# Kernel tuning notes

Hardware: AMD Instinct MI355X
Metric: run time of the kernel (lower is better)

The kernel has to match this reference:

```python
import jax, jax.numpy as jnp
import numpy as np

K = 3
PAD = 1

def conv2d(x, w, b=None):
    # x: [B,C,H,W], w: [O,C,kh,kw], stride 1, padding 1
    y = jax.lax.conv_general_dilated(x, w, (1, 1), [(PAD, PAD), (PAD, PAD)],
                                     dimension_numbers=('NCHW', 'OIHW', 'NCHW'))
    if b is not None:
        y = y + b[None, :, None, None]
    return y

def deform_conv2d(x, offset, mask, w):
    # Faithful torchvision DeformConv2d (v2, stride=1, dilation=1, pad=1, no bias).
    # x: [B,C,H,W]; offset: [B,2*K*K,H,W] with (dy,dx) interleaved per kernel pt;
    # mask: [B,K*K,H,W]; w: [O,C,K,K]
    B, C, H, W = x.shape
    KK = K * K
    off = offset.reshape(B, KK, 2, H, W)
    offs_y, offs_x = off[:, :, 0], off[:, :, 1]           # [B,KK,H,W]
    ky = (jnp.arange(KK) // K).astype(jnp.float32) - PAD   # kernel row offsets
    kx = (jnp.arange(KK) % K).astype(jnp.float32) - PAD    # kernel col offsets
    py = offs_y + jnp.arange(H, dtype=jnp.float32)[None, None, :, None] + ky[None, :, None, None]
    px = offs_x + jnp.arange(W, dtype=jnp.float32)[None, None, None, :] + kx[None, :, None, None]
    y0f = jnp.floor(py); x0f = jnp.floor(px)
    wy = py - y0f; wx = px - x0f                           # bilinear fractions
    y0 = y0f.astype(jnp.int32); x0 = x0f.astype(jnp.int32)
    xf = x.reshape(B, C, H * W)

    def corner(yi, xi):
        valid = ((yi >= 0) & (yi < H) & (xi >= 0) & (xi < W)).astype(x.dtype)
        idx = jnp.clip(yi, 0, H - 1) * W + jnp.clip(xi, 0, W - 1)   # [B,KK,H,W]
        g = jax.vmap(lambda img, ix: img[:, ix])(xf, idx.reshape(B, KK * H * W))
        return g.reshape(B, C, KK, H, W) * valid[:, None]

    one = jnp.asarray(1.0, x.dtype)
    samp = (corner(y0, x0)         * ((one - wy) * (one - wx))[:, None]
          + corner(y0, x0 + 1)     * ((one - wy) * wx)[:, None]
          + corner(y0 + 1, x0)     * (wy * (one - wx))[:, None]
          + corner(y0 + 1, x0 + 1) * (wy * wx)[:, None])       # [B,C,KK,H,W]
    if mask is not None:
        samp = samp * mask[:, None]
    O = w.shape[0]
    return jnp.einsum('bckhw,ock->bohw', samp, w.reshape(O, C, KK))

def setup_inputs() -> dict:
    key = jax.random.key(0)
    ks = jax.random.split(key, 7)
    B, C, O, H, W = 4, 64, 64, 128, 128
    x = jax.random.normal(ks[0], (B, C, H, W), jnp.float32)
    ele = jax.random.normal(ks[1], (B, 1, H, W), jnp.float32)
    offset_w = jax.random.normal(ks[2], (2 * K * K, 1, 3, 3), jnp.float32) * 0.1
    offset_b = jnp.zeros((2 * K * K,), jnp.float32)
    mask_w = jax.random.normal(ks[3], (K * K, C, 3, 3), jnp.float32) * (1.0 / np.sqrt(C * 9))
    mask_b = jnp.zeros((K * K,), jnp.float32)
    deform_w = jax.random.normal(ks[4], (O, C, K, K), jnp.float32) * (1.0 / np.sqrt(C * 9))
    return {"x": x, "ele": ele, "offset_w": offset_w, "offset_b": offset_b,
            "mask_w": mask_w, "mask_b": mask_b, "deform_w": deform_w}

def reference(x, ele, offset_w, offset_b, mask_w, mask_b, deform_w):
    offset = conv2d(ele, offset_w, offset_b)                 # [B,18,H,W]
    mask = jax.nn.sigmoid(conv2d(x, mask_w, mask_b))         # [B,9,H,W]
    out = deform_conv2d(x, offset, mask, deform_w)           # [B,O,H,W]
    return jax.nn.relu(out)
```

## Files before the change

### kernel.cpp

```cpp
#include <hip/hip_runtime.h>
#include <hip/hip_bf16.h>
#include <hip/hip_fp16.h>

typedef _Float16 half8 __attribute__((ext_vector_type(8)));
typedef _Float16 half2v __attribute__((ext_vector_type(2)));
typedef float f32x4 __attribute__((ext_vector_type(4)));

#define B_ 4
#define C_ 64
#define O_ 64
#define H_ 128
#define W_ 128
#define HT 8
#define WT 16
#define HALO 3
#define RS 14
#define CS 22

__device__ __forceinline__ unsigned pkh(float lo, float hi) {
  half2v v = {(_Float16)lo, (_Float16)hi};
  return __builtin_bit_cast(unsigned, v);
}

__global__ void build_frags(const float* __restrict__ dw,
                            const float* __restrict__ mw,
                            _Float16* __restrict__ wsb) {
  int t = blockIdx.x * 256 + threadIdx.x;
  if (t < 36864) {
    int j = t & 7, lane = (t >> 3) & 63, ot = (t >> 9) & 3, s = t >> 11;
    int kk = s >> 1, ch = s & 1;
    int o = ot * 16 + (lane & 15);
    int c = ch * 32 + ((lane >> 4) << 3) + j;
    wsb[t] = (_Float16)dw[(o * 64 + c) * 9 + kk];
  } else if (t < 46080) {
    int t2 = t - 36864;
    int j = t2 & 7, lane = (t2 >> 3) & 63, s = t2 >> 9;
    int km = lane & 15;
    int c = (s & 1) * 32 + ((lane >> 4) << 3) + j;
    int tap = s >> 1;
    float v = (km < 9) ? mw[(km * 64 + c) * 9 + tap] : 0.0f;
    wsb[t] = (_Float16)v;
  }
}

__global__ __launch_bounds__(512, 4)
void deform_main(const float* __restrict__ x,
                 const float* __restrict__ ele,
                 const float* __restrict__ ow,
                 const float* __restrict__ ob,
                 const float* __restrict__ mb,
                 const _Float16* __restrict__ wsb,
                 float* __restrict__ out) {
  __shared__ uint4 xs4[RS * CS * 9];
  __shared__ _Float16 offl[128 * 18];
  __shared__ _Float16 maskl[128 * 9];
  __shared__ uint2 cwb[128 * 9];
  __shared__ unsigned crc[128 * 9];

  const int tid = threadIdx.x;
  const int lane = tid & 63;
  const int wv = tid >> 6;
  const int pcl = lane & 15;
  const int lq = lane >> 4;

  const int bid = blockIdx.x;
  const int d = ((bid & 7) << 6) + (bid >> 3);
  const int b = d >> 7;
  const int t7 = d & 127;
  const int r0 = (t7 >> 3) * HT;
  const int c0 = (t7 & 7) * WT;

  float ev[9];
  {
    int tl = tid & 127;
    int pr = tl >> 4, pc = tl & 15;
    int h = r0 + pr, w = c0 + pc;
#pragma unroll
    for (int ty = 0; ty < 3; ++ty)
#pragma unroll
      for (int tx = 0; tx < 3; ++tx) {
        int gy = h - 1 + ty, gx = w - 1 + tx;
        float v = 0.0f;
        if ((unsigned)gy < 128u && (unsigned)gx < 128u)
          v = ele[b * (H_ * W_) + (gy << 7) + gx];
        ev[ty * 3 + tx] = v;
      }
  }

  {
    _Float16* xsb = (_Float16*)xs4;
    const int c2 = tid >> 4;
    const int pl = tid & 15;
    const float* xb0 = x + b * (C_ * H_ * W_) + (2 * c2) * (H_ * W_);
    const float* xb1 = xb0 + (H_ * W_);
    for (int p = pl; p < RS * CS; p += 16) {
      int row = (p * 2979) >> 16;
      int col = p - row * CS;
      int gy = r0 - HALO + row, gx = c0 - HALO + col;
      float v0 = 0.0f, v1 = 0.0f;
      if ((unsigned)gy < 128u && (unsigned)gx < 128u) {
        int gi = (gy << 7) + gx;
        v0 = xb0[gi];
        v1 = xb1[gi];
      }
      half2v hv = {(_Float16)v0, (_Float16)v1};
      *(half2v*)&xsb[p * 72 + 2 * c2] = hv;
    }
  }

  if (tid < 128) {
#pragma unroll
    for (int ci = 0; ci < 18; ++ci) {
      float a = ob[ci];
#pragma unroll
      for (int tap = 0; tap < 9; ++tap) a += ev[tap] * ow[ci * 9 + tap];
      offl[tid * 18 + ci] = (_Float16)a;
    }
  }
  __syncthreads();

  {
    const half8* wfm8 = ((const half8*)wsb) + 4608;
    f32x4 macc = {0.f, 0.f, 0.f, 0.f};
#pragma unroll
    for (int s = 0; s < 18; ++s) {
      const int tap = s >> 1;
      const int chalf = s & 1;
      const int ty = tap / 3, tx = tap - ty * 3;
      half8 aw = wfm8[s * 64 + lane];
      const int csl = chalf * 4 + lq;
      int rc = (wv + (HALO - 1) + ty) * CS + (pcl + (HALO - 1) + tx);
      half8 xv = *(const half8*)(xs4 + rc * 9 + csl);
      macc = __builtin_amdgcn_mfma_f32_16x16x32_f16(aw, xv, macc, 0, 0, 0);
    }
    int px = wv * 16 + pcl;
#pragma unroll
    for (int r = 0; r < 4; ++r) {
      int km = lq * 4 + r;
      if (km < 9) {
        float a = macc[r] + mb[km];
        float m = 1.0f / (1.0f + __expf(-a));
        maskl[px * 9 + km] = (_Float16)m;
      }
    }
  }
  __syncthreads();

  for (int it = tid; it < 128 * 9; it += 512) {
    int px = (it * 7282) >> 16;
    int kk = it - px * 9;
    int pr = px >> 4, pc = px & 15;
    int h = r0 + pr, w = c0 + pc;
    int ky = kk / 3 - 1;
    int kx = kk - (kk / 3) * 3 - 1;
    half2v o2 = *(const half2v*)&offl[px * 18 + kk * 2];
    float m = (float)maskl[px * 9 + kk];
    float py = (float)(h + ky) + (float)o2[0];
    float pxx = (float)(w + kx) + (float)o2[1];
    float fy = floorf(py), fx = floorf(pxx);
    float wy = py - fy, wx = pxx - fx;
    int iy = (int)fy - r0 + HALO;
    int ix = (int)fx - c0 + HALO;
    int vy0 = (unsigned)iy < (unsigned)RS;
    int vy1 = (unsigned)(iy + 1) < (unsigned)RS;
    int vx0 = (unsigned)ix < (unsigned)CS;
    int vx1 = (unsigned)(ix + 1) < (unsigned)CS;
    int cy0 = min(max(iy, 0), RS - 1), cy1 = min(max(iy + 1, 0), RS - 1);
    int cx0 = min(max(ix, 0), CS - 1), cx1 = min(max(ix + 1, 0), CS - 1);
    float wy0 = 1.0f - wy, wx0 = 1.0f - wx;
    float a00 = wy0 * wx0 * m * (float)(vy0 & vx0);
    float a01 = wy0 * wx * m * (float)(vy0 & vx1);
    float a10 = wy * wx0 * m * (float)(vy1 & vx0);
    float a11 = wy * wx * m * (float)(vy1 & vx1);
    int rc00 = cy0 * CS + cx0;
    int drow = (cy1 - cy0) * CS;
    int dcol = cx1 - cx0;
    uint2 cv;
    cv.x = pkh(a00, a01);
    cv.y = pkh(a10, a11);
    cwb[it] = cv;
    crc[it] = (unsigned)rc00 | ((unsigned)drow << 16) | ((unsigned)dcol << 24);
  }
  __syncthreads();

  const half8* wf8 = (const half8*)wsb;
  f32x4 acc[4];
#pragma unroll
  for (int ot = 0; ot < 4; ++ot) {
    f32x4 z = {0.f, 0.f, 0.f, 0.f};
    acc[ot] = z;
  }

  const int px = wv * 16 + pcl;
  const int h = r0 + wv;
  const int w = c0 + pcl;

#pragma unroll
  for (int kk = 0; kk < 9; ++kk) {
    uint2 cv = cwb[px * 9 + kk];
    unsigned rv = crc[px * 9 + kk];
    int rc00 = rv & 0xFFFF;
    int drow = (rv >> 16) & 0xFF;
    int dcol = rv >> 24;
    int rc01 = rc00 + dcol;
    int rc10 = rc00 + drow;
    int rc11 = rc10 + dcol;
    half2v c01 = __builtin_bit_cast(half2v, cv.x);
    half2v c23 = __builtin_bit_cast(half2v, cv.y);
    _Float16 a00 = c01[0], a01 = c01[1], a10 = c23[0], a11 = c23[1];
    half8 a00s = {a00, a00, a00, a00, a00, a00, a00, a00};
    half8 a01s = {a01, a01, a01, a01, a01, a01, a01, a01};
    half8 a10s = {a10, a10, a10, a10, a10, a10, a10, a10};
    half8 a11s = {a11, a11, a11, a11, a11, a11, a11, a11};
#pragma unroll
    for (int ch = 0; ch < 2; ++ch) {
      const int csl = ch * 4 + lq;
      half8 v00 = *(const half8*)(xs4 + rc00 * 9 + csl);
      half8 v01 = *(const half8*)(xs4 + rc01 * 9 + csl);
      half8 v10 = *(const half8*)(xs4 + rc10 * 9 + csl);
      half8 v11 = *(const half8*)(xs4 + rc11 * 9 + csl);
      half8 t = v00 * a00s + v01 * a01s + v10 * a10s + v11 * a11s;
      const int sidx = kk * 2 + ch;
#pragma unroll
      for (int ot = 0; ot < 4; ++ot) {
        half8 bw = wf8[(sidx * 4 + ot) * 64 + lane];
        acc[ot] = __builtin_amdgcn_mfma_f32_16x16x32_f16(bw, t, acc[ot], 0, 0, 0);
      }
    }
  }

#pragma unroll
  for (int ot = 0; ot < 4; ++ot) {
#pragma unroll
    for (int r = 0; r < 4; ++r) {
      int o = ot * 16 + lq * 4 + r;
      float v = fmaxf(acc[ot][r], 0.0f);
      out[((b * O_ + o) << 14) + (h << 7) + w] = v;
    }
  }
}

extern "C" void kernel_launch(void* const* d_in, const int* in_sizes, int n_in,
                              void* d_out, int out_size, void* d_ws, size_t ws_size,
                              hipStream_t stream) {
  const float* x   = (const float*)d_in[0];
  const float* ele = (const float*)d_in[1];
  const float* ow  = (const float*)d_in[2];
  const float* ob  = (const float*)d_in[3];
  const float* mw  = (const float*)d_in[4];
  const float* mb  = (const float*)d_in[5];
  const float* dw  = (const float*)d_in[6];
  _Float16* wsb = (_Float16*)d_ws;

  build_frags<<<180, 256, 0, stream>>>(dw, mw, wsb);
  deform_main<<<512, 512, 0, stream>>>(x, ele, ow, ob, mb, wsb,
                                       (float*)d_out);
}
```

Baseline: 32.29 us.

## Fuse mask sigmoid into bilinear coefficient setup and prefetch weight fragments

Spreads the offset convolution over all 512 threads (4 threads per pixel, each computing a strided subset of the 18 channels) instead of only 128. The mask MFMA epilogue now computes the bilinear corner coefficients directly from the sigmoid in registers, which removes the maskl shared buffer, one barrier and a separate loop. In the main loop, weight fragments for the next step are loaded one step ahead into registers, and s_setprio raises priority around the MFMAs. This costs extra registers under the 512-thread launch bound, and the coefficient work is now limited to 9 of 16 lanes per column group. A leftover empty loop does nothing.

```diff
diff --git a/kernel.cpp b/kernel.cpp
--- a/kernel.cpp
+++ b/kernel.cpp
@@ -53,7 +53,6 @@
                  float* __restrict__ out) {
   __shared__ uint4 xs4[RS * CS * 9];
   __shared__ _Float16 offl[128 * 18];
-  __shared__ _Float16 maskl[128 * 9];
   __shared__ uint2 cwb[128 * 9];
   __shared__ unsigned crc[128 * 9];
 
@@ -72,8 +71,8 @@
 
   float ev[9];
   {
-    int tl = tid & 127;
-    int pr = tl >> 4, pc = tl & 15;
+    int px = tid >> 2;
+    int pr = px >> 4, pc = px & 15;
     int h = r0 + pr, w = c0 + pc;
 #pragma unroll
     for (int ty = 0; ty < 3; ++ty)
@@ -108,13 +107,22 @@
     }
   }
 
-  if (tid < 128) {
+  {
+    int px = tid >> 2;
+    int g = tid & 3;
 #pragma unroll
     for (int ci = 0; ci < 18; ++ci) {
-      float a = ob[ci];
-#pragma unroll
-      for (int tap = 0; tap < 9; ++tap) a += ev[tap] * ow[ci * 9 + tap];
-      offl[tid * 18 + ci] = (_Float16)a;
+      if ((ci & 3) == 0 || (ci - g) % 4 == 0) {}
+    }
+#pragma unroll
+    for (int k5 = 0; k5 < 5; ++k5) {
+      int ci = g + k5 * 4;
+      if (ci < 18) {
+        float a = ob[ci];
+#pragma unroll
+        for (int tap = 0; tap < 9; ++tap) a += ev[tap] * ow[ci * 9 + tap];
+        offl[px * 18 + ci] = (_Float16)a;
+      }
     }
   }
   __syncthreads();
@@ -134,52 +142,44 @@
       macc = __builtin_amdgcn_mfma_f32_16x16x32_f16(aw, xv, macc, 0, 0, 0);
     }
     int px = wv * 16 + pcl;
+    int h = r0 + wv, w = c0 + pcl;
 #pragma unroll
     for (int r = 0; r < 4; ++r) {
-      int km = lq * 4 + r;
-      if (km < 9) {
-        float a = macc[r] + mb[km];
+      int kk = lq * 4 + r;
+      if (kk < 9) {
+        float a = macc[r] + mb[kk];
         float m = 1.0f / (1.0f + __expf(-a));
-        maskl[px * 9 + km] = (_Float16)m;
-      }
-    }
-  }
-  __syncthreads();
-
-  for (int it = tid; it < 128 * 9; it += 512) {
-    int px = (it * 7282) >> 16;
-    int kk = it - px * 9;
-    int pr = px >> 4, pc = px & 15;
-    int h = r0 + pr, w = c0 + pc;
-    int ky = kk / 3 - 1;
-    int kx = kk - (kk / 3) * 3 - 1;
-    half2v o2 = *(const half2v*)&offl[px * 18 + kk * 2];
-    float m = (float)maskl[px * 9 + kk];
-    float py = (float)(h + ky) + (float)o2[0];
-    float pxx = (float)(w + kx) + (float)o2[1];
-    float fy = floorf(py), fx = floorf(pxx);
-    float wy = py - fy, wx = pxx - fx;
-    int iy = (int)fy - r0 + HALO;
-    int ix = (int)fx - c0 + HALO;
-    int vy0 = (unsigned)iy < (unsigned)RS;
-    int vy1 = (unsigned)(iy + 1) < (unsigned)RS;
-    int vx0 = (unsigned)ix < (unsigned)CS;
-    int vx1 = (unsigned)(ix + 1) < (unsigned)CS;
-    int cy0 = min(max(iy, 0), RS - 1), cy1 = min(max(iy + 1, 0), RS - 1);
-    int cx0 = min(max(ix, 0), CS - 1), cx1 = min(max(ix + 1, 0), CS - 1);
-    float wy0 = 1.0f - wy, wx0 = 1.0f - wx;
-    float a00 = wy0 * wx0 * m * (float)(vy0 & vx0);
-    float a01 = wy0 * wx * m * (float)(vy0 & vx1);
-    float a10 = wy * wx0 * m * (float)(vy1 & vx0);
-    float a11 = wy * wx * m * (float)(vy1 & vx1);
-    int rc00 = cy0 * CS + cx0;
-    int drow = (cy1 - cy0) * CS;
-    int dcol = cx1 - cx0;
-    uint2 cv;
-    cv.x = pkh(a00, a01);
-    cv.y = pkh(a10, a11);
-    cwb[it] = cv;
-    crc[it] = (unsigned)rc00 | ((unsigned)drow << 16) | ((unsigned)dcol << 24);
+        int ky = kk / 3 - 1;
+        int kx = kk - (kk / 3) * 3 - 1;
+        half2v o2 = *(const half2v*)&offl[px * 18 + kk * 2];
+        float py = (float)(h + ky) + (float)o2[0];
+        float pxx = (float)(w + kx) + (float)o2[1];
+        float fy = floorf(py), fx = floorf(pxx);
+        float wy = py - fy, wx = pxx - fx;
+        int iy = (int)fy - r0 + HALO;
+        int ix = (int)fx - c0 + HALO;
+        int vy0 = (unsigned)iy < (unsigned)RS;
+        int vy1 = (unsigned)(iy + 1) < (unsigned)RS;
+        int vx0 = (unsigned)ix < (unsigned)CS;
+        int vx1 = (unsigned)(ix + 1) < (unsigned)CS;
+        int cy0 = min(max(iy, 0), RS - 1), cy1 = min(max(iy + 1, 0), RS - 1);
+        int cx0 = min(max(ix, 0), CS - 1), cx1 = min(max(ix + 1, 0), CS - 1);
+        float wy0 = 1.0f - wy, wx0 = 1.0f - wx;
+        float a00 = wy0 * wx0 * m * (float)(vy0 & vx0);
+        float a01 = wy0 * wx * m * (float)(vy0 & vx1);
+        float a10 = wy * wx0 * m * (float)(vy1 & vx0);
+        float a11 = wy * wx * m * (float)(vy1 & vx1);
+        int rc00 = cy0 * CS + cx0;
+        int drow = (cy1 - cy0) * CS;
+        int dcol = cx1 - cx0;
+        uint2 cv;
+        cv.x = pkh(a00, a01);
+        cv.y = pkh(a10, a11);
+        cwb[px * 9 + kk] = cv;
+        crc[px * 9 + kk] = (unsigned)rc00 | ((unsigned)drow << 16) |
+                           ((unsigned)dcol << 24);
+      }
+    }
   }
   __syncthreads();
 
@@ -192,8 +192,10 @@
   }
 
   const int px = wv * 16 + pcl;
-  const int h = r0 + wv;
-  const int w = c0 + pcl;
+
+  half8 bwbuf[4];
+#pragma unroll
+  for (int ot = 0; ot < 4; ++ot) bwbuf[ot] = wf8[ot * 64 + lane];
 
 #pragma unroll
   for (int kk = 0; kk < 9; ++kk) {
@@ -219,16 +221,28 @@
       half8 v01 = *(const half8*)(xs4 + rc01 * 9 + csl);
       half8 v10 = *(const half8*)(xs4 + rc10 * 9 + csl);
       half8 v11 = *(const half8*)(xs4 + rc11 * 9 + csl);
+      const int nsidx = kk * 2 + ch + 1;
+      half8 bwn[4];
+      if (nsidx < 18) {
+#pragma unroll
+        for (int ot = 0; ot < 4; ++ot)
+          bwn[ot] = wf8[(nsidx * 4 + ot) * 64 + lane];
+      }
       half8 t = v00 * a00s + v01 * a01s + v10 * a10s + v11 * a11s;
-      const int sidx = kk * 2 + ch;
-#pragma unroll
-      for (int ot = 0; ot < 4; ++ot) {
-        half8 bw = wf8[(sidx * 4 + ot) * 64 + lane];
-        acc[ot] = __builtin_amdgcn_mfma_f32_16x16x32_f16(bw, t, acc[ot], 0, 0, 0);
-      }
-    }
-  }
-
+      __builtin_amdgcn_s_setprio(1);
+#pragma unroll
+      for (int ot = 0; ot < 4; ++ot)
+        acc[ot] = __builtin_amdgcn_mfma_f32_16x16x32_f16(bwbuf[ot], t, acc[ot], 0, 0, 0);
+      __builtin_amdgcn_s_setprio(0);
+      if (nsidx < 18) {
+#pragma unroll
+        for (int ot = 0; ot < 4; ++ot) bwbuf[ot] = bwn[ot];
+      }
+    }
+  }
+
+  const int h = r0 + wv;
+  const int w = c0 + pcl;
 #pragma unroll
   for (int ot = 0; ot < 4; ++ot) {
 #pragma unroll
```

Result: slower. 33.39 us (+3.4%).

## Split fused deform kernel into coefficient and GEMM kernels via global workspace

Applied to the files above, without the earlier changes.

The single fused kernel is split into two launches. A coefficient kernel computes the mask and bilinear coefficients directly from the mask MFMA outputs and writes them to global workspace. A GEMM kernel then reloads those coefficients into registers and reruns the halo load of x before the deformable MFMA loop. This removes two barriers and some shared-memory use from each kernel, which may improve occupancy. The cost is an extra launch, a second load of the x tile, and a global round-trip of the coefficients.

```diff
diff --git a/kernel.cpp b/kernel.cpp
--- a/kernel.cpp
+++ b/kernel.cpp
@@ -16,6 +16,9 @@
 #define HALO 3
 #define RS 14
 #define CS 22
+
+#define CWG_OFF 92160
+#define CRG_OFF (92160 + 512 * 1152 * 8)
 
 __device__ __forceinline__ unsigned pkh(float lo, float hi) {
   half2v v = {(_Float16)lo, (_Float16)hi};
@@ -44,18 +47,16 @@
 }
 
 __global__ __launch_bounds__(512, 4)
-void deform_main(const float* __restrict__ x,
+void coef_kernel(const float* __restrict__ x,
                  const float* __restrict__ ele,
                  const float* __restrict__ ow,
                  const float* __restrict__ ob,
                  const float* __restrict__ mb,
                  const _Float16* __restrict__ wsb,
-                 float* __restrict__ out) {
+                 uint2* __restrict__ cwg,
+                 unsigned* __restrict__ crg) {
   __shared__ uint4 xs4[RS * CS * 9];
   __shared__ _Float16 offl[128 * 18];
-  __shared__ _Float16 maskl[128 * 9];
-  __shared__ uint2 cwb[128 * 9];
-  __shared__ unsigned crc[128 * 9];
 
   const int tid = threadIdx.x;
   const int lane = tid & 63;
@@ -133,53 +134,111 @@
       half8 xv = *(const half8*)(xs4 + rc * 9 + csl);
       macc = __builtin_amdgcn_mfma_f32_16x16x32_f16(aw, xv, macc, 0, 0, 0);
     }
-    int px = wv * 16 + pcl;
+    const int px = wv * 16 + pcl;
+    const int h = r0 + wv, w = c0 + pcl;
+    const long cbase = (long)d * 1152;
 #pragma unroll
     for (int r = 0; r < 4; ++r) {
-      int km = lq * 4 + r;
-      if (km < 9) {
-        float a = macc[r] + mb[km];
+      int kk = lq * 4 + r;
+      if (kk < 9) {
+        float a = macc[r] + mb[kk];
         float m = 1.0f / (1.0f + __expf(-a));
-        maskl[px * 9 + km] = (_Float16)m;
+        int ky = kk / 3 - 1;
+        int kx = kk - (kk / 3) * 3 - 1;
+        half2v o2 = *(const half2v*)&offl[px * 18 + kk * 2];
+        float py = (float)(h + ky) + (float)o2[0];
+        float pxx = (float)(w + kx) + (float)o2[1];
+        float fy = floorf(py), fx = floorf(pxx);
+        float wy = py - fy, wx = pxx - fx;
+        int iy = (int)fy - r0 + HALO;
+        int ix = (int)fx - c0 + HALO;
+        int vy0 = (unsigned)iy < (unsigned)RS;
+        int vy1 = (unsigned)(iy + 1) < (unsigned)RS;
+        int vx0 = (unsigned)ix < (unsigned)CS;
+        int vx1 = (unsigned)(ix + 1) < (unsigned)CS;
+        int cy0 = min(max(iy, 0), RS - 1), cy1 = min(max(iy + 1, 0), RS - 1);
+        int cx0 = min(max(ix, 0), CS - 1), cx1 = min(max(ix + 1, 0), CS - 1);
+        float wy0 = 1.0f - wy, wx0 = 1.0f - wx;
+        float a00 = wy0 * wx0 * m * (float)(vy0 & vx0);
+        float a01 = wy0 * wx * m * (float)(vy0 & vx1);
+        float a10 = wy * wx0 * m * (float)(vy1 & vx0);
+        float a11 = wy * wx * m * (float)(vy1 & vx1);
+        int rc00 = cy0 * CS + cx0;
+        int drow = (cy1 - cy0) * CS;
+        int dcol = cx1 - cx0;
+        uint2 cv;
+        cv.x = pkh(a00, a01);
+        cv.y = pkh(a10, a11);
+        cwg[cbase + kk * 128 + px] = cv;
+        crg[cbase + kk * 128 + px] =
+            (unsigned)rc00 | ((unsigned)drow << 16) | ((unsigned)dcol << 24);
       }
     }
   }
-  __syncthreads();
-
-  for (int it = tid; it < 128 * 9; it += 512) {
-    int px = (it * 7282) >> 16;
-    int kk = it - px * 9;
-    int pr = px >> 4, pc = px & 15;
-    int h = r0 + pr, w = c0 + pc;
-    int ky = kk / 3 - 1;
-    int kx = kk - (kk / 3) * 3 - 1;
-    half2v o2 = *(const half2v*)&offl[px * 18 + kk * 2];
-    float m = (float)maskl[px * 9 + kk];
-    float py = (float)(h + ky) + (float)o2[0];
-    float pxx = (float)(w + kx) + (float)o2[1];
-    float fy = floorf(py), fx = floorf(pxx);
-    float wy = py - fy, wx = pxx - fx;
-    int iy = (int)fy - r0 + HALO;
-    int ix = (int)fx - c0 + HALO;
-    int vy0 = (unsigned)iy < (unsigned)RS;
-    int vy1 = (unsigned)(iy + 1) < (unsigned)RS;
-    int vx0 = (unsigned)ix < (unsigned)CS;
-    int vx1 = (unsigned)(ix + 1) < (unsigned)CS;
-    int cy0 = min(max(iy, 0), RS - 1), cy1 = min(max(iy + 1, 0), RS - 1);
-    int cx0 = min(max(ix, 0), CS - 1), cx1 = min(max(ix + 1, 0), CS - 1);
-    float wy0 = 1.0f - wy, wx0 = 1.0f - wx;
-    float a00 = wy0 * wx0 * m * (float)(vy0 & vx0);
-    float a01 = wy0 * wx * m * (float)(vy0 & vx1);
-    float a10 = wy * wx0 * m * (float)(vy1 & vx0);
-    float a11 = wy * wx * m * (float)(vy1 & vx1);
-    int rc00 = cy0 * CS + cx0;
-    int drow = (cy1 - cy0) * CS;
-    int dcol = cx1 - cx0;
-    uint2 cv;
-    cv.x = pkh(a00, a01);
-    cv.y = pkh(a10, a11);
-    cwb[it] = cv;
-    crc[it] = (unsigned)rc00 | ((unsigned)drow << 16) | ((unsigned)dcol << 24);
+}
+
+__global__ __launch_bounds__(512, 4)
+void gemm_kernel(const float* __restrict__ x,
+                 const _Float16* __restrict__ wsb,
+                 const uint2* __restrict__ cwg,
+                 const unsigned* __restrict__ crg,
+                 float* __restrict__ out) {
+  __shared__ uint4 xs4[RS * CS * 9];
+
+  const int tid = threadIdx.x;
+  const int lane = tid & 63;
+  const int wv = tid >> 6;
+  const int pcl = lane & 15;
+  const int lq = lane >> 4;
+
+  const int bid = blockIdx.x;
+  const int d = ((bid & 7) << 6) + (bid >> 3);
+  const int b = d >> 7;
+  const int t7 = d & 127;
+  const int r0 = (t7 >> 3) * HT;
+  const int c0 = (t7 & 7) * WT;
+
+  const int px = wv * 16 + pcl;
+
+  const long cbase = (long)d * 1152 + px;
+  uint2 cv0 = cwg[cbase + 0 * 128];
+  uint2 cv1 = cwg[cbase + 1 * 128];
+  uint2 cv2 = cwg[cbase + 2 * 128];
+  uint2 cv3 = cwg[cbase + 3 * 128];
+  uint2 cv4 = cwg[cbase + 4 * 128];
+  uint2 cv5 = cwg[cbase + 5 * 128];
+  uint2 cv6 = cwg[cbase + 6 * 128];
+  uint2 cv7 = cwg[cbase + 7 * 128];
+  uint2 cv8 = cwg[cbase + 8 * 128];
+  unsigned rv0 = crg[cbase + 0 * 128];
+  unsigned rv1 = crg[cbase + 1 * 128];
+  unsigned rv2 = crg[cbase + 2 * 128];
+  unsigned rv3 = crg[cbase + 3 * 128];
+  unsigned rv4 = crg[cbase + 4 * 128];
+  unsigned rv5 = crg[cbase + 5 * 128];
+  unsigned rv6 = crg[cbase + 6 * 128];
+  unsigned rv7 = crg[cbase + 7 * 128];
+  unsigned rv8 = crg[cbase + 8 * 128];
+
+  {
+    _Float16* xsb = (_Float16*)xs4;
+    const int c2 = tid >> 4;
+    const int pl = tid & 15;
+    const float* xb0 = x + b * (C_ * H_ * W_) + (2 * c2) * (H_ * W_);
+    const float* xb1 = xb0 + (H_ * W_);
+    for (int p = pl; p < RS * CS; p += 16) {
+      int row = (p * 2979) >> 16;
+      int col = p - row * CS;
+      int gy = r0 - HALO + row, gx = c0 - HALO + col;
+      float v0 = 0.0f, v1 = 0.0f;
+      if ((unsigned)gy < 128u && (unsigned)gx < 128u) {
+        int gi = (gy << 7) + gx;
+        v0 = xb0[gi];
+        v1 = xb1[gi];
+      }
+      half2v hv = {(_Float16)v0, (_Float16)v1};
+      *(half2v*)&xsb[p * 72 + 2 * c2] = hv;
+    }
   }
   __syncthreads();
 
@@ -191,44 +250,52 @@
     acc[ot] = z;
   }
 
-  const int px = wv * 16 + pcl;
+#define KKSTEP(KK, CV, RV)                                                   \
+  {                                                                          \
+    int rc00 = (RV)&0xFFFF;                                                  \
+    int drow = ((RV) >> 16) & 0xFF;                                          \
+    int dcol = (RV) >> 24;                                                   \
+    int rc01 = rc00 + dcol;                                                  \
+    int rc10 = rc00 + drow;                                                  \
+    int rc11 = rc10 + dcol;                                                  \
+    half2v c01 = __builtin_bit_cast(half2v, (CV).x);                         \
+    half2v c23 = __builtin_bit_cast(half2v, (CV).y);                         \
+    _Float16 a00 = c01[0], a01 = c01[1], a10 = c23[0], a11 = c23[1];         \
+    half8 a00s = {a00, a00, a00, a00, a00, a00, a00, a00};                   \
+    half8 a01s = {a01, a01, a01, a01, a01, a01, a01, a01};                   \
+    half8 a10s = {a10, a10, a10, a10, a10, a10, a10, a10};                   \
+    half8 a11s = {a11, a11, a11, a11, a11, a11, a11, a11};                   \
+    _Pragma("unroll")                                                        \
+    for (int ch = 0; ch < 2; ++ch) {                                         \
+      const int csl = ch * 4 + lq;                                           \
+      half8 v00 = *(const half8*)(xs4 + rc00 * 9 + csl);                     \
+      half8 v01 = *(const half8*)(xs4 + rc01 * 9 + csl);                     \
+      half8 v10 = *(const half8*)(xs4 + rc10 * 9 + csl);                     \
+      half8 v11 = *(const half8*)(xs4 + rc11 * 9 + csl);                     \
+      half8 t = v00 * a00s + v01 * a01s + v10 * a10s + v11 * a11s;           \
+      const int sidx = (KK)*2 + ch;                                          \
+      _Pragma("unroll")                                                      \
+      for (int ot = 0; ot < 4; ++ot) {                                       \
+        half8 bw = wf8[(sidx * 4 + ot) * 64 + lane];                         \
+        acc[ot] =                                                            \
+            __builtin_amdgcn_mfma_f32_16x16x32_f16(bw, t, acc[ot], 0, 0, 0); \
+      }                                                                      \
+    }                                                                        \
+  }
+
+  KKSTEP(0, cv0, rv0)
+  KKSTEP(1, cv1, rv1)
+  KKSTEP(2, cv2, rv2)
+  KKSTEP(3, cv3, rv3)
+  KKSTEP(4, cv4, rv4)
+  KKSTEP(5, cv5, rv5)
+  KKSTEP(6, cv6, rv6)
+  KKSTEP(7, cv7, rv7)
+  KKSTEP(8, cv8, rv8)
+#undef KKSTEP
+
   const int h = r0 + wv;
   const int w = c0 + pcl;
-
-#pragma unroll
-  for (int kk = 0; kk < 9; ++kk) {
-    uint2 cv = cwb[px * 9 + kk];
-    unsigned rv = crc[px * 9 + kk];
-    int rc00 = rv & 0xFFFF;
-    int drow = (rv >> 16) & 0xFF;
-    int dcol = rv >> 24;
-    int rc01 = rc00 + dcol;
-    int rc10 = rc00 + drow;
-    int rc11 = rc10 + dcol;
-    half2v c01 = __builtin_bit_cast(half2v, cv.x);
-    half2v c23 = __builtin_bit_cast(half2v, cv.y);
-    _Float16 a00 = c01[0], a01 = c01[1], a10 = c23[0], a11 = c23[1];
-    half8 a00s = {a00, a00, a00, a00, a00, a00, a00, a00};
-    half8 a01s = {a01, a01, a01, a01, a01, a01, a01, a01};
-    half8 a10s = {a10, a10, a10, a10, a10, a10, a10, a10};
-    half8 a11s = {a11, a11, a11, a11, a11, a11, a11, a11};
-#pragma unroll
-    for (int ch = 0; ch < 2; ++ch) {
-      const int csl = ch * 4 + lq;
-      half8 v00 = *(const half8*)(xs4 + rc00 * 9 + csl);
-      half8 v01 = *(const half8*)(xs4 + rc01 * 9 + csl);
-      half8 v10 = *(const half8*)(xs4 + rc10 * 9 + csl);
-      half8 v11 = *(const half8*)(xs4 + rc11 * 9 + csl);
-      half8 t = v00 * a00s + v01 * a01s + v10 * a10s + v11 * a11s;
-      const int sidx = kk * 2 + ch;
-#pragma unroll
-      for (int ot = 0; ot < 4; ++ot) {
-        half8 bw = wf8[(sidx * 4 + ot) * 64 + lane];
-        acc[ot] = __builtin_amdgcn_mfma_f32_16x16x32_f16(bw, t, acc[ot], 0, 0, 0);
-      }
-    }
-  }
-
 #pragma unroll
   for (int ot = 0; ot < 4; ++ot) {
 #pragma unroll
@@ -251,8 +318,10 @@
   const float* mb  = (const float*)d_in[5];
   const float* dw  = (const float*)d_in[6];
   _Float16* wsb = (_Float16*)d_ws;
+  uint2* cwg = (uint2*)((char*)d_ws + CWG_OFF);
+  unsigned* crg = (unsigned*)((char*)d_ws + CRG_OFF);
 
   build_frags<<<180, 256, 0, stream>>>(dw, mw, wsb);
-  deform_main<<<512, 512, 0, stream>>>(x, ele, ow, ob, mb, wsb,
-                                       (float*)d_out);
-}
+  coef_kernel<<<512, 512, 0, stream>>>(x, ele, ow, ob, mb, wsb, cwg, crg);
+  gemm_kernel<<<512, 512, 0, stream>>>(x, wsb, cwg, crg, (float*)d_out);
+}
```

New measurement: 42.58 us. 31.9% more time.
